# Kernel optimization log

Measured on AMD Instinct MI355X. Metric: run time of the kernel, lower is better.

The kernel has to match this reference:

```python
import jax, jax.numpy as jnp
import numpy as np

N_NODES = 50000
N_EDGES = 800000
IN_FEATS = 64
OUT_FEATS = 64
EDGE_DIM = 8


def setup_inputs() -> dict:
    key = jax.random.key(0)
    k1, k2, k3, k4, k5 = jax.random.split(key, 5)
    node_feat = jax.random.normal(k1, (N_NODES, IN_FEATS), dtype=jnp.float32)
    edge_feat = jax.random.normal(k2, (N_EDGES, EDGE_DIM), dtype=jnp.float32)
    W = jax.random.normal(k3, (OUT_FEATS, IN_FEATS), dtype=jnp.float32) * (1.0 / np.sqrt(IN_FEATS))
    b = jnp.zeros((OUT_FEATS,), dtype=jnp.float32)
    src = jax.random.randint(k4, (N_EDGES,), 0, N_NODES, dtype=jnp.int64 if jax.config.jax_enable_x64 else jnp.int32)
    dst = jax.random.randint(k5, (N_EDGES,), 0, N_NODES, dtype=jnp.int64 if jax.config.jax_enable_x64 else jnp.int32)
    return {"node_feat": node_feat, "edge_feat": edge_feat, "W": W, "b": b,
            "src": src, "dst": dst}


def reference(node_feat, edge_feat, W, b, src, dst):
    # EfConv forward with aggregate='sum', node_feat.shape[1] == in_feats.
    n_nodes = node_feat.shape[0]
    edge_dim = edge_feat.shape[1]
    h_src = node_feat[src]  # [E, in_feats] gather once, reused for every slice
    aggs = []
    for k in range(edge_dim):  # small fixed loop over edge feature slices
        m = h_src * edge_feat[:, k:k + 1]                      # u_mul_e: [E, in_feats]
        aggs.append(jax.ops.segment_sum(m, dst, num_segments=n_nodes))
    agg = jnp.stack(aggs, axis=1)                              # [N, edge_dim, in_feats]
    # per-slice shared linear, then concat along feature dim
    out = jnp.einsum('nki,oi->nko', agg, W) + b                # [N, edge_dim, out_feats]
    return out.reshape(n_nodes, edge_dim * W.shape[0])         # [N, edge_dim*out_feats]
```

## Files before the change

### kernel.cpp

```cpp
#include <hip/hip_runtime.h>


#define FEATS 64
#define EDGE_DIM 8

__global__ void __launch_bounds__(256) transform_kernel(
    const float* __restrict__ nf, const float* __restrict__ W,
    float* __restrict__ t, int n_nodes)
{
    __shared__ float sWt[FEATS * 65];
    __shared__ float srow[4][FEATS];
    const int tid = threadIdx.x;

    #pragma unroll
    for (int base = 0; base < FEATS * FEATS; base += 256) {
        int idx = base + tid;
        int o = idx >> 6;
        int i = idx & 63;
        sWt[i * 65 + o] = W[idx];
    }

    const int r = tid >> 6;
    const int o = tid & 63;
    const int node = blockIdx.x * 4 + r;
    if (node < n_nodes) srow[r][o] = nf[(long)node * FEATS + o];
    __syncthreads();

    if (node >= n_nodes) return;
    float sum = 0.f;
    #pragma unroll
    for (int i = 0; i < FEATS; i++)
        sum += srow[r][i] * sWt[i * 65 + o];
    t[(long)node * FEATS + o] = sum;
}

__global__ void __launch_bounds__(256) zero_kernel(int* __restrict__ p, int n)
{
    int i = blockIdx.x * 256 + threadIdx.x;
    if (i < n) p[i] = 0;
}

__global__ void __launch_bounds__(256) hist_kernel(
    const int* __restrict__ dst, int* __restrict__ deg, int n_edges)
{
    int e = blockIdx.x * 256 + threadIdx.x;
    if (e < n_edges) atomicAdd(&deg[dst[e]], 1);
}

__global__ void __launch_bounds__(256) partials_kernel(
    const int* __restrict__ deg, int* __restrict__ partials, int n)
{
    __shared__ int s[256];
    int i = blockIdx.x * 256 + threadIdx.x;
    s[threadIdx.x] = (i < n) ? deg[i] : 0;
    __syncthreads();
    for (int off = 128; off > 0; off >>= 1) {
        if (threadIdx.x < off) s[threadIdx.x] += s[threadIdx.x + off];
        __syncthreads();
    }
    if (threadIdx.x == 0) partials[blockIdx.x] = s[0];
}

__global__ void __launch_bounds__(256) scan_partials_kernel(
    const int* __restrict__ partials, int* __restrict__ pscan, int nb)
{
    __shared__ int s[256];
    int tid = threadIdx.x;
    s[tid] = (tid < nb) ? partials[tid] : 0;
    for (int off = 1; off < 256; off <<= 1) {
        __syncthreads();
        int x = (tid >= off) ? s[tid - off] : 0;
        __syncthreads();
        s[tid] += x;
    }
    __syncthreads();
    pscan[tid] = (tid == 0) ? 0 : s[tid - 1];
}

__global__ void __launch_bounds__(256) scan_addback_kernel(
    const int* __restrict__ deg, const int* __restrict__ pscan,
    int* __restrict__ offsets, int* __restrict__ cursor,
    int n, int n_edges)
{
    __shared__ int s[256];
    int tid = threadIdx.x;
    int i = blockIdx.x * 256 + tid;
    int v = (i < n) ? deg[i] : 0;
    s[tid] = v;
    for (int off = 1; off < 256; off <<= 1) {
        __syncthreads();
        int x = (tid >= off) ? s[tid - off] : 0;
        __syncthreads();
        s[tid] += x;
    }
    __syncthreads();
    if (i < n) {
        int excl = pscan[blockIdx.x] + s[tid] - v;
        offsets[i] = excl;
        cursor[i]  = excl;
    }
    if (blockIdx.x == 0 && tid == 0) offsets[n] = n_edges;
}

__global__ void __launch_bounds__(256) permute_kernel(
    const int* __restrict__ src, const int* __restrict__ dst,
    int* __restrict__ cursor, int* __restrict__ src_s, int* __restrict__ perm,
    int n_edges)
{
    int e = blockIdx.x * 256 + threadIdx.x;
    if (e >= n_edges) return;
    int pos = atomicAdd(&cursor[dst[e]], 1);
    src_s[pos] = src[e];
    perm[pos] = e;
}

__global__ void __launch_bounds__(256) aggregate_kernel(
    const float* __restrict__ t, const float* __restrict__ ef,
    const int* __restrict__ src_s, const int* __restrict__ perm,
    const int* __restrict__ offsets, const float* __restrict__ b,
    float* __restrict__ out, int n_nodes)
{
    int node = (blockIdx.x * 256 + threadIdx.x) >> 6;
    int o = threadIdx.x & 63;
    if (node >= n_nodes) return;

    int beg = offsets[node];
    int end = offsets[node + 1];
    float acc[EDGE_DIM];
    #pragma unroll
    for (int k = 0; k < EDGE_DIM; k++) acc[k] = 0.f;

    int j = beg;
    for (; j + 1 < end; j += 2) {
        int e0 = perm[j],     e1 = perm[j + 1];
        int s0 = src_s[j],    s1 = src_s[j + 1];
        float tv0 = t[(long)s0 * FEATS + o];
        float tv1 = t[(long)s1 * FEATS + o];
        const float4* p0 = (const float4*)(ef + (long)e0 * EDGE_DIM);
        const float4* p1 = (const float4*)(ef + (long)e1 * EDGE_DIM);
        float4 a0 = p0[0], a1 = p0[1];
        float4 c0 = p1[0], c1 = p1[1];
        acc[0] += a0.x * tv0; acc[1] += a0.y * tv0;
        acc[2] += a0.z * tv0; acc[3] += a0.w * tv0;
        acc[4] += a1.x * tv0; acc[5] += a1.y * tv0;
        acc[6] += a1.z * tv0; acc[7] += a1.w * tv0;
        acc[0] += c0.x * tv1; acc[1] += c0.y * tv1;
        acc[2] += c0.z * tv1; acc[3] += c0.w * tv1;
        acc[4] += c1.x * tv1; acc[5] += c1.y * tv1;
        acc[6] += c1.z * tv1; acc[7] += c1.w * tv1;
    }
    if (j < end) {
        int e0 = perm[j];
        int s0 = src_s[j];
        float tv0 = t[(long)s0 * FEATS + o];
        const float4* p0 = (const float4*)(ef + (long)e0 * EDGE_DIM);
        float4 a0 = p0[0], a1 = p0[1];
        acc[0] += a0.x * tv0; acc[1] += a0.y * tv0;
        acc[2] += a0.z * tv0; acc[3] += a0.w * tv0;
        acc[4] += a1.x * tv0; acc[5] += a1.y * tv0;
        acc[6] += a1.z * tv0; acc[7] += a1.w * tv0;
    }

    float bo = b[o];
    float* op = out + (long)node * (EDGE_DIM * FEATS) + o;
    #pragma unroll
    for (int k = 0; k < EDGE_DIM; k++)
        op[k * FEATS] = acc[k] + bo;
}

extern "C" void kernel_launch(void* const* d_in, const int* in_sizes, int n_in,
                              void* d_out, int out_size, void* d_ws, size_t ws_size,
                              hipStream_t stream) {
    const float* node_feat = (const float*)d_in[0];
    const float* edge_feat = (const float*)d_in[1];
    const float* W         = (const float*)d_in[2];
    const float* b         = (const float*)d_in[3];
    const int*   src       = (const int*)d_in[4];
    const int*   dst       = (const int*)d_in[5];
    float* out = (float*)d_out;

    const int n_nodes = in_sizes[0] / FEATS;
    const int n_edges = in_sizes[4];
    const int nb_nodes = (n_nodes + 255) / 256;
    const int nb_edges = (n_edges + 255) / 256;

    int* w = (int*)d_ws;
    float* t      = (float*)w;
    int* deg      = w + (long)n_nodes * FEATS;
    int* offsets  = deg + n_nodes;
    int* cursor   = offsets + n_nodes + 1;
    int* partials = cursor + n_nodes;
    int* pscan    = partials + 256;
    int* src_s    = pscan + 256;
    int* perm     = src_s + n_edges;

    transform_kernel<<<(n_nodes + 3) / 4, 256, 0, stream>>>(node_feat, W, t, n_nodes);
    zero_kernel<<<nb_nodes, 256, 0, stream>>>(deg, n_nodes);
    hist_kernel<<<nb_edges, 256, 0, stream>>>(dst, deg, n_edges);
    partials_kernel<<<nb_nodes, 256, 0, stream>>>(deg, partials, n_nodes);
    scan_partials_kernel<<<1, 256, 0, stream>>>(partials, pscan, nb_nodes);
    scan_addback_kernel<<<nb_nodes, 256, 0, stream>>>(deg, pscan, offsets, cursor,
                                                      n_nodes, n_edges);
    permute_kernel<<<nb_edges, 256, 0, stream>>>(src, dst, cursor, src_s, perm, n_edges);

    const long total_ag = (long)n_nodes * 64;
    aggregate_kernel<<<(int)((total_ag + 255) / 256), 256, 0, stream>>>(
        t, edge_feat, src_s, perm, offsets, b, out, n_nodes);
}
```

Measured before the change: 335.4 us.

## Fuse degree zeroing, vectorize edge passes, pack src/perm pairs, unroll aggregation

```diff
diff --git a/kernel.cpp b/kernel.cpp
--- a/kernel.cpp
+++ b/kernel.cpp
@@ -6,11 +6,14 @@
 
 __global__ void __launch_bounds__(256) transform_kernel(
     const float* __restrict__ nf, const float* __restrict__ W,
-    float* __restrict__ t, int n_nodes)
+    float* __restrict__ t, int* __restrict__ deg, int n_nodes)
 {
     __shared__ float sWt[FEATS * 65];
     __shared__ float srow[4][FEATS];
     const int tid = threadIdx.x;
+
+    int gid = blockIdx.x * 256 + tid;
+    if (gid < n_nodes) deg[gid] = 0;
 
     #pragma unroll
     for (int base = 0; base < FEATS * FEATS; base += 256) {
@@ -34,17 +37,19 @@
     t[(long)node * FEATS + o] = sum;
 }
 
-__global__ void __launch_bounds__(256) zero_kernel(int* __restrict__ p, int n)
-{
-    int i = blockIdx.x * 256 + threadIdx.x;
-    if (i < n) p[i] = 0;
-}
-
 __global__ void __launch_bounds__(256) hist_kernel(
     const int* __restrict__ dst, int* __restrict__ deg, int n_edges)
 {
-    int e = blockIdx.x * 256 + threadIdx.x;
-    if (e < n_edges) atomicAdd(&deg[dst[e]], 1);
+    int i4 = (blockIdx.x * 256 + threadIdx.x) * 4;
+    if (i4 + 3 < n_edges) {
+        int4 d = *(const int4*)(dst + i4);
+        atomicAdd(&deg[d.x], 1);
+        atomicAdd(&deg[d.y], 1);
+        atomicAdd(&deg[d.z], 1);
+        atomicAdd(&deg[d.w], 1);
+    } else {
+        for (int e = i4; e < n_edges; ++e) atomicAdd(&deg[dst[e]], 1);
+    }
 }
 
 __global__ void __launch_bounds__(256) partials_kernel(
@@ -104,68 +109,83 @@
 
 __global__ void __launch_bounds__(256) permute_kernel(
     const int* __restrict__ src, const int* __restrict__ dst,
-    int* __restrict__ cursor, int* __restrict__ src_s, int* __restrict__ perm,
-    int n_edges)
-{
-    int e = blockIdx.x * 256 + threadIdx.x;
-    if (e >= n_edges) return;
-    int pos = atomicAdd(&cursor[dst[e]], 1);
-    src_s[pos] = src[e];
-    perm[pos] = e;
-}
+    int* __restrict__ cursor, int2* __restrict__ pairs, int n_edges)
+{
+    int i4 = (blockIdx.x * 256 + threadIdx.x) * 4;
+    if (i4 + 3 < n_edges) {
+        int4 s = *(const int4*)(src + i4);
+        int4 d = *(const int4*)(dst + i4);
+        int p;
+        p = atomicAdd(&cursor[d.x], 1); pairs[p] = make_int2(s.x, i4 + 0);
+        p = atomicAdd(&cursor[d.y], 1); pairs[p] = make_int2(s.y, i4 + 1);
+        p = atomicAdd(&cursor[d.z], 1); pairs[p] = make_int2(s.z, i4 + 2);
+        p = atomicAdd(&cursor[d.w], 1); pairs[p] = make_int2(s.w, i4 + 3);
+    } else {
+        for (int e = i4; e < n_edges; ++e) {
+            int p = atomicAdd(&cursor[dst[e]], 1);
+            pairs[p] = make_int2(src[e], e);
+        }
+    }
+}
+
+#define FMA8(A0, A1, TV)                                \
+    acc[0] += A0.x * TV; acc[1] += A0.y * TV;           \
+    acc[2] += A0.z * TV; acc[3] += A0.w * TV;           \
+    acc[4] += A1.x * TV; acc[5] += A1.y * TV;           \
+    acc[6] += A1.z * TV; acc[7] += A1.w * TV;
 
 __global__ void __launch_bounds__(256) aggregate_kernel(
     const float* __restrict__ t, const float* __restrict__ ef,
-    const int* __restrict__ src_s, const int* __restrict__ perm,
-    const int* __restrict__ offsets, const float* __restrict__ b,
-    float* __restrict__ out, int n_nodes)
-{
-    int node = (blockIdx.x * 256 + threadIdx.x) >> 6;
-    int o = threadIdx.x & 63;
+    const int2* __restrict__ pairs, const int* __restrict__ offsets,
+    const float* __restrict__ b, float* __restrict__ out, int n_nodes)
+{
+    const int node = __builtin_amdgcn_readfirstlane(
+        (int)((blockIdx.x * 256 + threadIdx.x) >> 6));
+    const int o = threadIdx.x & 63;
     if (node >= n_nodes) return;
 
-    int beg = offsets[node];
-    int end = offsets[node + 1];
+    const int beg = offsets[node];
+    const int end = offsets[node + 1];
     float acc[EDGE_DIM];
     #pragma unroll
     for (int k = 0; k < EDGE_DIM; k++) acc[k] = 0.f;
 
     int j = beg;
-    for (; j + 1 < end; j += 2) {
-        int e0 = perm[j],     e1 = perm[j + 1];
-        int s0 = src_s[j],    s1 = src_s[j + 1];
-        float tv0 = t[(long)s0 * FEATS + o];
-        float tv1 = t[(long)s1 * FEATS + o];
-        const float4* p0 = (const float4*)(ef + (long)e0 * EDGE_DIM);
-        const float4* p1 = (const float4*)(ef + (long)e1 * EDGE_DIM);
-        float4 a0 = p0[0], a1 = p0[1];
-        float4 c0 = p1[0], c1 = p1[1];
-        acc[0] += a0.x * tv0; acc[1] += a0.y * tv0;
-        acc[2] += a0.z * tv0; acc[3] += a0.w * tv0;
-        acc[4] += a1.x * tv0; acc[5] += a1.y * tv0;
-        acc[6] += a1.z * tv0; acc[7] += a1.w * tv0;
-        acc[0] += c0.x * tv1; acc[1] += c0.y * tv1;
-        acc[2] += c0.z * tv1; acc[3] += c0.w * tv1;
-        acc[4] += c1.x * tv1; acc[5] += c1.y * tv1;
-        acc[6] += c1.z * tv1; acc[7] += c1.w * tv1;
-    }
-    if (j < end) {
-        int e0 = perm[j];
-        int s0 = src_s[j];
-        float tv0 = t[(long)s0 * FEATS + o];
-        const float4* p0 = (const float4*)(ef + (long)e0 * EDGE_DIM);
-        float4 a0 = p0[0], a1 = p0[1];
-        acc[0] += a0.x * tv0; acc[1] += a0.y * tv0;
-        acc[2] += a0.z * tv0; acc[3] += a0.w * tv0;
-        acc[4] += a1.x * tv0; acc[5] += a1.y * tv0;
-        acc[6] += a1.z * tv0; acc[7] += a1.w * tv0;
-    }
-
-    float bo = b[o];
+    for (; j + 3 < end; j += 4) {
+        int2 p0 = pairs[j];
+        int2 p1 = pairs[j + 1];
+        int2 p2 = pairs[j + 2];
+        int2 p3 = pairs[j + 3];
+        float tv0 = t[(long)p0.x * FEATS + o];
+        float tv1 = t[(long)p1.x * FEATS + o];
+        float tv2 = t[(long)p2.x * FEATS + o];
+        float tv3 = t[(long)p3.x * FEATS + o];
+        const float4* q0 = (const float4*)(ef + (long)p0.y * EDGE_DIM);
+        const float4* q1 = (const float4*)(ef + (long)p1.y * EDGE_DIM);
+        const float4* q2 = (const float4*)(ef + (long)p2.y * EDGE_DIM);
+        const float4* q3 = (const float4*)(ef + (long)p3.y * EDGE_DIM);
+        float4 a0 = q0[0], a1 = q0[1];
+        float4 b0 = q1[0], b1 = q1[1];
+        float4 c0 = q2[0], c1 = q2[1];
+        float4 d0 = q3[0], d1 = q3[1];
+        FMA8(a0, a1, tv0)
+        FMA8(b0, b1, tv1)
+        FMA8(c0, c1, tv2)
+        FMA8(d0, d1, tv3)
+    }
+    for (; j < end; ++j) {
+        int2 p = pairs[j];
+        float tv = t[(long)p.x * FEATS + o];
+        const float4* q = (const float4*)(ef + (long)p.y * EDGE_DIM);
+        float4 a0 = q[0], a1 = q[1];
+        FMA8(a0, a1, tv)
+    }
+
+    const float bo = b[o];
     float* op = out + (long)node * (EDGE_DIM * FEATS) + o;
     #pragma unroll
     for (int k = 0; k < EDGE_DIM; k++)
-        op[k * FEATS] = acc[k] + bo;
+        __builtin_nontemporal_store(acc[k] + bo, op + k * FEATS);
 }
 
 extern "C" void kernel_launch(void* const* d_in, const int* in_sizes, int n_in,
@@ -182,7 +202,7 @@
     const int n_nodes = in_sizes[0] / FEATS;
     const int n_edges = in_sizes[4];
     const int nb_nodes = (n_nodes + 255) / 256;
-    const int nb_edges = (n_edges + 255) / 256;
+    const int nb_e4    = (n_edges + 1023) / 1024;
 
     int* w = (int*)d_ws;
     float* t      = (float*)w;
@@ -191,19 +211,19 @@
     int* cursor   = offsets + n_nodes + 1;
     int* partials = cursor + n_nodes;
     int* pscan    = partials + 256;
-    int* src_s    = pscan + 256;
-    int* perm     = src_s + n_edges;
-
-    transform_kernel<<<(n_nodes + 3) / 4, 256, 0, stream>>>(node_feat, W, t, n_nodes);
-    zero_kernel<<<nb_nodes, 256, 0, stream>>>(deg, n_nodes);
-    hist_kernel<<<nb_edges, 256, 0, stream>>>(dst, deg, n_edges);
+    uintptr_t paddr = (uintptr_t)(pscan + 256);
+    paddr = (paddr + 7) & ~(uintptr_t)7;
+    int2* pairs   = (int2*)paddr;
+
+    transform_kernel<<<(n_nodes + 3) / 4, 256, 0, stream>>>(node_feat, W, t, deg, n_nodes);
+    hist_kernel<<<nb_e4, 256, 0, stream>>>(dst, deg, n_edges);
     partials_kernel<<<nb_nodes, 256, 0, stream>>>(deg, partials, n_nodes);
     scan_partials_kernel<<<1, 256, 0, stream>>>(partials, pscan, nb_nodes);
     scan_addback_kernel<<<nb_nodes, 256, 0, stream>>>(deg, pscan, offsets, cursor,
                                                       n_nodes, n_edges);
-    permute_kernel<<<nb_edges, 256, 0, stream>>>(src, dst, cursor, src_s, perm, n_edges);
+    permute_kernel<<<nb_e4, 256, 0, stream>>>(src, dst, cursor, pairs, n_edges);
 
     const long total_ag = (long)n_nodes * 64;
     aggregate_kernel<<<(int)((total_ag + 255) / 256), 256, 0, stream>>>(
-        t, edge_feat, src_s, perm, offsets, b, out, n_nodes);
-}
+        t, edge_feat, pairs, offsets, b, out, n_nodes);
+}
```

Result: faster. 319.8 us (-4.7%).
